# Kernel optimization log

Hardware: AMD Instinct MI355X
Metric: run time of the kernel (lower is better)

Reference implementation:

```python
import jax, jax.numpy as jnp
import numpy as np

N_NODES = 50000
N_EDGES = 800000
N_GRAPHS = 64
IN_DIM = 128
HID = 64
HEADS = 4
LAT = 32
BN_EPS = 1e-5


def setup_inputs() -> dict:
    key = jax.random.key(0)
    ks = jax.random.split(key, 16)
    x = jax.random.normal(ks[0], (N_NODES, IN_DIM), jnp.float32)
    edge_index = jax.random.randint(ks[1], (2, N_EDGES), 0, N_NODES, dtype=jnp.int64)
    batch = jnp.sort(jax.random.randint(ks[2], (N_NODES,), 0, N_GRAPHS, dtype=jnp.int64))

    def lin(k, fan_in, shape):
        return (jax.random.normal(k, shape, jnp.float32) / np.sqrt(fan_in)).astype(jnp.float32)

    d = {"x": x, "edge_index": edge_index, "batch": batch}
    dims = [IN_DIM, HID, HID]
    i = 3
    for l, din in enumerate(dims):
        d[f"Wl{l}"] = lin(ks[i], din, (din, HEADS * HID)); i += 1
        d[f"Wr{l}"] = lin(ks[i], din, (din, HEADS * HID)); i += 1
        d[f"att{l}"] = lin(ks[i], HID, (HEADS, HID)); i += 1
        d[f"b{l}"] = jnp.zeros((HID,), jnp.float32)
    d["bn_gamma"] = jnp.ones((HID,), jnp.float32)
    d["bn_beta"] = jnp.zeros((HID,), jnp.float32)
    d["fc_W"] = lin(ks[i], HID, (LAT, HID)); i += 1
    d["fc_b"] = jnp.zeros((LAT,), jnp.float32)
    return d


def _gatv2_conv(x, Wl, Wr, att, b, src, dst):
    # PyG GATv2Conv, concat=False: mean over heads. src -> dst message flow.
    n = x.shape[0]
    H, D = att.shape
    xl = (x @ Wl).reshape(n, H, D)   # source-side transform
    xr = (x @ Wr).reshape(n, H, D)   # target-side transform
    e = jax.nn.leaky_relu(xl[src] + xr[dst], 0.2)        # [E, H, D]
    logits = jnp.einsum('ehd,hd->eh', e, att)            # [E, H]
    # segment softmax over incoming edges of each dst node
    m = jax.ops.segment_max(logits, dst, num_segments=n)
    p = jnp.exp(logits - m[dst])
    denom = jax.ops.segment_sum(p, dst, num_segments=n)
    alpha = p / (denom[dst] + 1e-16)                     # [E, H]
    out = jax.ops.segment_sum(alpha[..., None] * xl[src], dst, num_segments=n)  # [N, H, D]
    return out.mean(axis=1) + b


def reference(x, edge_index, batch, Wl0, Wr0, att0, b0, Wl1, Wr1, att1, b1,
              Wl2, Wr2, att2, b2, bn_gamma, bn_beta, fc_W, fc_b):
    src, dst = edge_index[0], edge_index[1]
    h = x
    for (Wl, Wr, att, b) in ((Wl0, Wr0, att0, b0), (Wl1, Wr1, att1, b1), (Wl2, Wr2, att2, b2)):
        h = _gatv2_conv(h, Wl, Wr, att, b, src, dst)
        h = jax.nn.leaky_relu(h, 0.1)
        # dropout omitted (deterministic reference / eval semantics)
    pooled = jax.ops.segment_sum(h, batch, num_segments=N_GRAPHS)  # [G, HID]
    mean = pooled.mean(axis=0)
    var = pooled.var(axis=0)  # biased variance, matches BN training normalization
    y = (pooled - mean) / jnp.sqrt(var + BN_EPS) * bn_gamma + bn_beta
    return y @ fc_W.T + fc_b
```

## Files before the change

kernel.cpp:

```cpp
#include <hip/hip_runtime.h>
#include <hip/hip_bf16.h>
#include <math.h>
#include <string.h>

#define N_NODES 50000
#define N_EDGES 800000
#define N_GRAPHS 64
#define IN_DIM 128
#define HID 64
#define HEADS 4
#define LAT 32
#define SCAN_BLOCKS ((N_NODES + 255) / 256)
#define ES_CAP 960000

typedef __attribute__((ext_vector_type(8))) short bf16x8;
typedef __attribute__((ext_vector_type(4))) float floatx4;
typedef __attribute__((ext_vector_type(2))) float f32x2;

__device__ inline unsigned short f2bf(float f) {
    unsigned u = __float_as_uint(f);
    return (unsigned short)((u + 0x7fffu + ((u >> 16) & 1u)) >> 16);
}

__device__ inline unsigned pkbf(float x, float y) {
    float2 f{x, y};
    __hip_bfloat162 h = __float22bfloat162_rn(f);
    unsigned u;
    memcpy(&u, &h, sizeof(u));
    return u;
}

__device__ inline f32x2 bfpair(unsigned u) {
    f32x2 r;
    r.x = __uint_as_float(u << 16);
    r.y = __uint_as_float(u & 0xffff0000u);
    return r;
}

__device__ inline float rowsum16(float x) {
    x += __int_as_float(__builtin_amdgcn_mov_dpp(__float_as_int(x), 0x128, 0xf, 0xf, false));
    x += __int_as_float(__builtin_amdgcn_mov_dpp(__float_as_int(x), 0x124, 0xf, 0xf, false));
    x += __int_as_float(__builtin_amdgcn_mov_dpp(__float_as_int(x), 0x122, 0xf, 0xf, false));
    x += __int_as_float(__builtin_amdgcn_mov_dpp(__float_as_int(x), 0x121, 0xf, 0xf, false));
    return x;
}

__global__ __launch_bounds__(256) void prep_kernel(
    const float* __restrict__ x, unsigned* __restrict__ xbf,
    const float* __restrict__ Wl0, const float* __restrict__ Wr0,
    const float* __restrict__ Wl1, const float* __restrict__ Wr1,
    const float* __restrict__ Wl2, const float* __restrict__ Wr2,
    unsigned short* __restrict__ B0, unsigned short* __restrict__ B1,
    unsigned short* __restrict__ B2,
    int* __restrict__ cnt, float* __restrict__ pooled, int* __restrict__ done,
    uint4* __restrict__ es4) {
    int b = blockIdx.x, t = threadIdx.x;
    if (b < 3072) {
        for (int i = b * 256 + t; i < N_NODES * IN_DIM / 2; i += 3072 * 256) {
            float2 v = reinterpret_cast<const float2*>(x)[i];
            xbf[i] = pkbf(v.x, v.y);
        }
    } else if (b < 3584) {
        int idx = (b - 3072) * 256 + t;
        const float *Wl, *Wr;
        unsigned short* B;
        int KC, local;
        if (idx < 65536)      { Wl = Wl0; Wr = Wr0; B = B0; KC = 4; local = idx; }
        else if (idx < 98304) { Wl = Wl1; Wr = Wr1; B = B1; KC = 2; local = idx - 65536; }
        else                  { Wl = Wl2; Wr = Wr2; B = B2; KC = 2; local = idx - 98304; }
        int j = local & 7;
        int lane = (local >> 3) & 63;
        int rem = local >> 9;
        int kc = rem % KC;
        int tile = rem / KC;
        int k = kc * 32 + (lane >> 4) * 8 + j;
        int tt = tile & 15;
        int n = (tt >> 3) * 128 + (lane & 15) * 8 + (tt & 7);
        const float* W = (tile < 16) ? Wl : Wr;
        B[local] = f2bf(W[k * 256 + n]);
    } else if (b < 3840) {
        int idx = (b - 3584) * 256 + t;
        if (idx < N_NODES) cnt[idx] = 0;
        if (idx < N_GRAPHS * HID) pooled[idx] = 0.f;
        if (idx == 0) *done = 0;
    } else {
        int idx = (b - 3840) * 256 + t;
        for (int i = idx; i < ES_CAP / 4; i += 65536)
            es4[i] = uint4{0, 0, 0, 0};
    }
}

__global__ __launch_bounds__(256) void deg_kernel(const int* __restrict__ dsts,
                                                  int* __restrict__ cnt, int E) {
    int e = blockIdx.x * 256 + threadIdx.x;
    if (e < E) atomicAdd(&cnt[dsts[e]], 1);
}

__global__ __launch_bounds__(256) void scan_kernel(const int* __restrict__ cnt,
                                                   int* __restrict__ offs,
                                                   int* __restrict__ sc,
                                                   int* __restrict__ agg) {
    __shared__ int buf[256];
    int b = blockIdx.x, t = threadIdx.x;
    int i = b * 256 + t;
    int v = (i < N_NODES) ? ((cnt[i] + 3) & ~3) : 0;
    buf[t] = v;
    __syncthreads();
    #pragma unroll
    for (int off = 1; off < 256; off <<= 1) {
        int tmp = (t >= off) ? buf[t - off] : 0;
        __syncthreads();
        buf[t] += tmp;
        __syncthreads();
    }
    int incl = buf[t];
    if (t == 255)
        __hip_atomic_store(&agg[b], buf[255] | 0x40000000,
                           __ATOMIC_RELEASE, __HIP_MEMORY_SCOPE_AGENT);
    int contrib = 0;
    if (t < b) {
        int vv;
        do {
            vv = __hip_atomic_load(&agg[t], __ATOMIC_ACQUIRE, __HIP_MEMORY_SCOPE_AGENT);
        } while (vv < 0 || !(vv & 0x40000000));
        contrib = vv & 0x3FFFFFFF;
    }
    __syncthreads();
    buf[t] = contrib;
    __syncthreads();
    for (int off = 128; off; off >>= 1) {
        if (t < off) buf[t] += buf[t + off];
        __syncthreads();
    }
    if (i < N_NODES) {
        offs[i] = buf[0] + incl - v;
        sc[i] = 0;
    }
}

__global__ __launch_bounds__(256) void scatter_kernel(const int* __restrict__ srcs,
                                                      const int* __restrict__ dsts,
                                                      const int* __restrict__ offs,
                                                      int* __restrict__ sc,
                                                      int* __restrict__ es, int E) {
    int e = blockIdx.x * 256 + threadIdx.x;
    if (e < E) {
        int d = dsts[e];
        int pos = offs[d] + atomicAdd(&sc[d], 1);
        es[pos] = srcs[e];
    }
}

template <int K>
__global__ __launch_bounds__(256) void gemm_mfma_kernel(
    const unsigned short* __restrict__ Abf,
    const unsigned short* __restrict__ Bpk,
    unsigned* __restrict__ xlp_u,
    unsigned* __restrict__ xrp_u) {
    constexpr int KC = K / 32;
    int br = blockIdx.x * 32;
    int t = threadIdx.x;
    int wave = t >> 6, lane = t & 63;
    int quad = lane >> 4, l16 = lane & 15;

    bf16x8 afrag[2][KC];
    #pragma unroll
    for (int rt = 0; rt < 2; ++rt) {
        int row = br + rt * 16 + l16;
        if (row > N_NODES - 1) row = N_NODES - 1;
        const unsigned short* ap = Abf + (size_t)row * K + quad * 8;
        #pragma unroll
        for (int kc = 0; kc < KC; ++kc)
            afrag[rt][kc] = *reinterpret_cast<const bf16x8*>(ap + kc * 32);
    }

    floatx4 acc[2][8];
    #pragma unroll
    for (int rt = 0; rt < 2; ++rt)
        #pragma unroll
        for (int i = 0; i < 8; ++i) acc[rt][i] = floatx4{0.f, 0.f, 0.f, 0.f};

    const bf16x8* bbase = reinterpret_cast<const bf16x8*>(Bpk)
                          + (size_t)(wave * 8) * KC * 64 + lane;
    #pragma unroll
    for (int i = 0; i < 8; ++i) {
        #pragma unroll
        for (int kc = 0; kc < KC; ++kc) {
            bf16x8 bfr = bbase[(i * KC + kc) * 64];
            acc[0][i] = __builtin_amdgcn_mfma_f32_16x16x32_bf16(afrag[0][kc], bfr, acc[0][i], 0, 0, 0);
            acc[1][i] = __builtin_amdgcn_mfma_f32_16x16x32_bf16(afrag[1][kc], bfr, acc[1][i], 0, 0, 0);
        }
    }

    unsigned* dst = (wave < 2) ? xlp_u : xrp_u;
    int cbase = (wave & 1) * 64 + l16 * 4;
    #pragma unroll
    for (int rt = 0; rt < 2; ++rt) {
        if (br + rt * 16 >= N_NODES) break;
        #pragma unroll
        for (int r = 0; r < 4; ++r) {
            int row = br + rt * 16 + quad * 4 + r;
            uint4 pk;
            pk.x = pkbf(acc[rt][0][r], acc[rt][1][r]);
            pk.y = pkbf(acc[rt][2][r], acc[rt][3][r]);
            pk.z = pkbf(acc[rt][4][r], acc[rt][5][r]);
            pk.w = pkbf(acc[rt][6][r], acc[rt][7][r]);
            *reinterpret_cast<uint4*>(&dst[(size_t)row * 128 + cbase]) = pk;
        }
    }
}

__global__ __launch_bounds__(256) void attn_kernel(const unsigned* __restrict__ xlp,
                                                   const unsigned* __restrict__ xrp,
                                                   const int* __restrict__ es,
                                                   const int* __restrict__ offs,
                                                   const int* __restrict__ deg,
                                                   const float4* __restrict__ att4,
                                                   const float4* __restrict__ bias4,
                                                   float* __restrict__ hout,
                                                   unsigned* __restrict__ hbf) {
    int node = blockIdx.x * 4 + (threadIdx.x >> 6);
    int lane = threadIdx.x & 63;
    int beg = offs[node];
    int end = beg + deg[node];
    uint2 xr2 = reinterpret_cast<const uint2*>(xrp)[(size_t)node * 64 + lane];
    f32x2 xrA = bfpair(xr2.x), xrB = bfpair(xr2.y);
    float4 at_t = att4[lane];
    f32x2 atA = {at_t.x, at_t.y}, atB = {at_t.z, at_t.w};
    const char* xbase = (const char*)xlp;
    int laneoff = lane << 3;

    float l = 0.f;
    f32x2 accA = {0.f, 0.f}, accB = {0.f, 0.f};

    auto edge_z = [&](uint2 v, f32x2& xa, f32x2& xb) -> float {
        xa = bfpair(v.x);
        xb = bfpair(v.y);
        f32x2 ea = xa + xrA;
        f32x2 eb = xb + xrB;
        ea = __builtin_elementwise_max(ea, ea * 0.2f);
        eb = __builtin_elementwise_max(eb, eb * 0.2f);
        f32x2 zz = ea * atA;
        zz += eb * atB;
        return zz.x + zz.y;
    };
    auto gather = [&](int s) -> uint2 {
        return *reinterpret_cast<const uint2*>(
            xbase + (((size_t)(unsigned)s) << 9) + laneoff);
    };

    for (int cb = beg; cb < end; cb += 4) {
        int4 s4 = *reinterpret_cast<const int4*>(&es[cb]);
        uint2 v0 = gather(s4.x);
        uint2 v1 = gather(s4.y);
        uint2 v2 = gather(s4.z);
        uint2 v3 = gather(s4.w);
        f32x2 xa0, xb0, xa1, xb1, xa2, xb2, xa3, xb3;
        float z0 = rowsum16(edge_z(v0, xa0, xb0));
        float z1 = rowsum16(edge_z(v1, xa1, xb1));
        float z2 = rowsum16(edge_z(v2, xa2, xb2));
        float z3 = rowsum16(edge_z(v3, xa3, xb3));
        float p0 = __expf(z0);
        float p1 = (cb + 1 < end) ? __expf(z1) : 0.f;
        float p2 = (cb + 2 < end) ? __expf(z2) : 0.f;
        float p3 = (cb + 3 < end) ? __expf(z3) : 0.f;
        accA += p0 * xa0 + p1 * xa1 + p2 * xa2 + p3 * xa3;
        accB += p0 * xb0 + p1 * xb1 + p2 * xb2 + p3 * xb3;
        l += (p0 + p1) + (p2 + p3);
    }

    float inv = 1.f / (l + 1e-16f);
    float a0 = accA.x * inv, a1 = accA.y * inv;
    float a2 = accB.x * inv, a3 = accB.y * inv;
    a0 += __shfl_xor(a0, 16); a0 += __shfl_xor(a0, 32);
    a1 += __shfl_xor(a1, 16); a1 += __shfl_xor(a1, 32);
    a2 += __shfl_xor(a2, 16); a2 += __shfl_xor(a2, 32);
    a3 += __shfl_xor(a3, 16); a3 += __shfl_xor(a3, 32);
    if (lane < 16) {
        float4 bv = bias4[lane];
        float4 o;
        o.x = 0.25f * a0 + bv.x; o.x = (o.x > 0.f) ? o.x : 0.1f * o.x;
        o.y = 0.25f * a1 + bv.y; o.y = (o.y > 0.f) ? o.y : 0.1f * o.y;
        o.z = 0.25f * a2 + bv.z; o.z = (o.z > 0.f) ? o.z : 0.1f * o.z;
        o.w = 0.25f * a3 + bv.w; o.w = (o.w > 0.f) ? o.w : 0.1f * o.w;
        if (hout)
            *reinterpret_cast<float4*>(&hout[(size_t)node * HID + lane * 4]) = o;
        if (hbf) {
            uint2 pk;
            pk.x = pkbf(o.x, o.y);
            pk.y = pkbf(o.z, o.w);
            *reinterpret_cast<uint2*>(&hbf[(size_t)node * 32 + lane * 2]) = pk;
        }
    }
}

__global__ __launch_bounds__(256) void pool_final_kernel(
    const float* __restrict__ hfin, const int* __restrict__ batch,
    float* __restrict__ pooled,
    const float* __restrict__ gamma, const float* __restrict__ beta,
    const float* __restrict__ fcW, const float* __restrict__ fcb,
    float* __restrict__ out, int* __restrict__ done) {
    int base = blockIdx.x * 256;
    int g = threadIdx.x >> 6, lane = threadIdx.x & 63;
    int lim = min(base + 256, N_NODES);
    int cur = -1;
    float s = 0.f;
    for (int i = base + g; i < lim; i += 4) {
        int b = batch[i];
        if (b != cur) {
            if (cur >= 0) atomicAdd(&pooled[cur * HID + lane], s);
            cur = b; s = 0.f;
        }
        s += hfin[(size_t)i * HID + lane];
    }
    if (cur >= 0) atomicAdd(&pooled[cur * HID + lane], s);

    __threadfence();
    __syncthreads();
    __shared__ int lastS;
    if (threadIdx.x == 0)
        lastS = (atomicAdd(done, 1) == (int)gridDim.x - 1);
    __syncthreads();
    if (!lastS) return;

    __shared__ float P[N_GRAPHS * HID];
    __shared__ float normS[N_GRAPHS * HID];
    __shared__ float meanS[HID], rstdS[HID];
    int t = threadIdx.x;
    for (int i = t; i < N_GRAPHS * HID; i += 256)
        P[i] = __hip_atomic_load(&pooled[i], __ATOMIC_RELAXED, __HIP_MEMORY_SCOPE_AGENT);
    __syncthreads();
    if (t < HID) {
        float s2 = 0.f;
        for (int g2 = 0; g2 < N_GRAPHS; ++g2) s2 += P[g2 * HID + t];
        float mean = s2 / (float)N_GRAPHS;
        float v = 0.f;
        for (int g2 = 0; g2 < N_GRAPHS; ++g2) {
            float dd = P[g2 * HID + t] - mean;
            v += dd * dd;
        }
        v /= (float)N_GRAPHS;
        meanS[t] = mean;
        rstdS[t] = rsqrtf(v + 1e-5f);
    }
    __syncthreads();
    for (int i = t; i < N_GRAPHS * HID; i += 256) {
        int d = i & 63;
        normS[i] = (P[i] - meanS[d]) * rstdS[d] * gamma[d] + beta[d];
    }
    __syncthreads();
    for (int i = t; i < N_GRAPHS * LAT; i += 256) {
        int g2 = i >> 5, lat = i & 31;
        float s2 = fcb[lat];
        for (int d = 0; d < HID; ++d) s2 += normS[g2 * HID + d] * fcW[lat * HID + d];
        out[i] = s2;
    }
}

extern "C" void kernel_launch(void* const* d_in, const int* in_sizes, int n_in,
                              void* d_out, int out_size, void* d_ws, size_t ws_size,
                              hipStream_t stream) {
    const float* x      = (const float*)d_in[0];
    const int*   ei     = (const int*)d_in[1];
    const int*   batch  = (const int*)d_in[2];
    const float* Wl[3]  = {(const float*)d_in[3], (const float*)d_in[7],  (const float*)d_in[11]};
    const float* Wr[3]  = {(const float*)d_in[4], (const float*)d_in[8],  (const float*)d_in[12]};
    const float* att[3] = {(const float*)d_in[5], (const float*)d_in[9],  (const float*)d_in[13]};
    const float* bia[3] = {(const float*)d_in[6], (const float*)d_in[10], (const float*)d_in[14]};
    const float* gamma  = (const float*)d_in[15];
    const float* beta   = (const float*)d_in[16];
    const float* fcW    = (const float*)d_in[17];
    const float* fcb    = (const float*)d_in[18];
    float* out = (float*)d_out;

    char* p = (char*)d_ws;
    auto alloc = [&](size_t bytes) {
        char* r = p;
        p += (bytes + 255) & ~(size_t)255;
        return r;
    };
    unsigned* xbf   = (unsigned*)alloc((size_t)N_NODES * IN_DIM * 2);
    unsigned* xlp   = (unsigned*)alloc((size_t)N_NODES * 256 * 2);
    unsigned* xrp   = (unsigned*)alloc((size_t)N_NODES * 256 * 2);
    unsigned* hbf0  = (unsigned*)alloc((size_t)N_NODES * HID * 2);
    unsigned* hbf1  = (unsigned*)alloc((size_t)N_NODES * HID * 2);
    unsigned short* Bpk0 = (unsigned short*)alloc(32 * 4 * 512 * 2);
    unsigned short* Bpk1 = (unsigned short*)alloc(32 * 2 * 512 * 2);
    unsigned short* Bpk2 = (unsigned short*)alloc(32 * 2 * 512 * 2);
    int*   es      = (int*)alloc((size_t)ES_CAP * 4);
    int*   offs    = (int*)alloc((size_t)N_NODES * 4);
    int*   cnt     = (int*)alloc((size_t)N_NODES * 4);
    int*   sc      = (int*)alloc((size_t)N_NODES * 4);
    int*   agg     = (int*)alloc((size_t)SCAN_BLOCKS * 4);
    int*   done    = (int*)alloc(256);
    float* pooled  = (float*)alloc((size_t)N_GRAPHS * HID * 4);
    float* hfin    = (float*)xbf;

    const int* srcs = ei;
    const int* dsts = ei + N_EDGES;

    prep_kernel<<<4096, 256, 0, stream>>>(x, xbf, Wl[0], Wr[0], Wl[1], Wr[1],
                                          Wl[2], Wr[2], Bpk0, Bpk1, Bpk2,
                                          cnt, pooled, done, (uint4*)es);
    int eb = (N_EDGES + 255) / 256;
    deg_kernel<<<eb, 256, 0, stream>>>(dsts, cnt, N_EDGES);
    scan_kernel<<<SCAN_BLOCKS, 256, 0, stream>>>(cnt, offs, sc, agg);
    scatter_kernel<<<eb, 256, 0, stream>>>(srcs, dsts, offs, sc, es, N_EDGES);

    int gb = (N_NODES + 31) / 32;
    gemm_mfma_kernel<IN_DIM><<<gb, 256, 0, stream>>>((const unsigned short*)xbf, Bpk0, xlp, xrp);
    attn_kernel<<<N_NODES / 4, 256, 0, stream>>>(xlp, xrp, es, offs, cnt,
                                                 (const float4*)att[0],
                                                 (const float4*)bia[0], nullptr, hbf0);
    gemm_mfma_kernel<HID><<<gb, 256, 0, stream>>>((const unsigned short*)hbf0, Bpk1, xlp, xrp);
    attn_kernel<<<N_NODES / 4, 256, 0, stream>>>(xlp, xrp, es, offs, cnt,
                                                 (const float4*)att[1],
                                                 (const float4*)bia[1], nullptr, hbf1);
    gemm_mfma_kernel<HID><<<gb, 256, 0, stream>>>((const unsigned short*)hbf1, Bpk2, xlp, xrp);
    attn_kernel<<<N_NODES / 4, 256, 0, stream>>>(xlp, xrp, es, offs, cnt,
                                                 (const float4*)att[2],
                                                 (const float4*)bia[2], hfin, nullptr);

    pool_final_kernel<<<SCAN_BLOCKS, 256, 0, stream>>>(hfin, batch, pooled,
                                                       gamma, beta, fcW, fcb,
                                                       out, done);
}
```

Baseline: 500.3 us.

## Stage GEMM A tile in LDS with 64-row blocks and vectorize edge kernels

The GEMM now processes 64 rows per 512-thread block, staging the A tile in shared memory so each wave reuses four row-tiles per B fragment load. The B packing and output column mapping change to match. Separately, the degree and scatter kernels read four edges per thread through int4 loads. This cuts redundant B-fragment global loads and per-edge load overhead, at the cost of more LDS use, a barrier, and more accumulator registers per thread.

After: 486.9 us. 2.7% less time.

```diff
diff --git a/kernel.cpp b/kernel.cpp
--- a/kernel.cpp
+++ b/kernel.cpp
@@ -75,7 +75,7 @@
         int tile = rem / KC;
         int k = kc * 32 + (lane >> 4) * 8 + j;
         int tt = tile & 15;
-        int n = (tt >> 3) * 128 + (lane & 15) * 8 + (tt & 7);
+        int n = (tt >> 2) * 64 + (lane & 15) * 4 + (tt & 3);
         const float* W = (tile < 16) ? Wl : Wr;
         B[local] = f2bf(W[k * 256 + n]);
     } else if (b < 3840) {
@@ -90,10 +90,16 @@
     }
 }
 
-__global__ __launch_bounds__(256) void deg_kernel(const int* __restrict__ dsts,
-                                                  int* __restrict__ cnt, int E) {
-    int e = blockIdx.x * 256 + threadIdx.x;
-    if (e < E) atomicAdd(&cnt[dsts[e]], 1);
+__global__ __launch_bounds__(256) void deg_kernel(const int4* __restrict__ dsts4,
+                                                  int* __restrict__ cnt, int E4) {
+    int i = blockIdx.x * 256 + threadIdx.x;
+    if (i < E4) {
+        int4 d = dsts4[i];
+        atomicAdd(&cnt[d.x], 1);
+        atomicAdd(&cnt[d.y], 1);
+        atomicAdd(&cnt[d.z], 1);
+        atomicAdd(&cnt[d.w], 1);
+    }
 }
 
 __global__ __launch_bounds__(256) void scan_kernel(const int* __restrict__ cnt,
@@ -138,74 +144,90 @@
     }
 }
 
-__global__ __launch_bounds__(256) void scatter_kernel(const int* __restrict__ srcs,
-                                                      const int* __restrict__ dsts,
+__global__ __launch_bounds__(256) void scatter_kernel(const int4* __restrict__ srcs4,
+                                                      const int4* __restrict__ dsts4,
                                                       const int* __restrict__ offs,
                                                       int* __restrict__ sc,
-                                                      int* __restrict__ es, int E) {
-    int e = blockIdx.x * 256 + threadIdx.x;
-    if (e < E) {
-        int d = dsts[e];
-        int pos = offs[d] + atomicAdd(&sc[d], 1);
-        es[pos] = srcs[e];
+                                                      int* __restrict__ es, int E4) {
+    int i = blockIdx.x * 256 + threadIdx.x;
+    if (i < E4) {
+        int4 s = srcs4[i];
+        int4 d = dsts4[i];
+        es[offs[d.x] + atomicAdd(&sc[d.x], 1)] = s.x;
+        es[offs[d.y] + atomicAdd(&sc[d.y], 1)] = s.y;
+        es[offs[d.z] + atomicAdd(&sc[d.z], 1)] = s.z;
+        es[offs[d.w] + atomicAdd(&sc[d.w], 1)] = s.w;
     }
 }
 
 template <int K>
-__global__ __launch_bounds__(256) void gemm_mfma_kernel(
+__global__ __launch_bounds__(512) void gemm_mfma_kernel(
     const unsigned short* __restrict__ Abf,
     const unsigned short* __restrict__ Bpk,
     unsigned* __restrict__ xlp_u,
     unsigned* __restrict__ xrp_u) {
     constexpr int KC = K / 32;
-    int br = blockIdx.x * 32;
+    constexpr int CHUNKS = 64 * K / 8;
+    __shared__ short As[CHUNKS * 8];
+    int br = blockIdx.x * 64;
     int t = threadIdx.x;
+
+    for (int c = t; c < CHUNKS; c += 512) {
+        int rt = c / (KC * 64);
+        int rem = c % (KC * 64);
+        int kc = rem >> 6;
+        int quad = (rem >> 4) & 3, l16 = rem & 15;
+        int row = br + rt * 16 + l16;
+        if (row >= N_NODES) row = N_NODES - 1;
+        *reinterpret_cast<uint4*>(&As[c * 8]) =
+            *reinterpret_cast<const uint4*>(&Abf[(size_t)row * K + kc * 32 + quad * 8]);
+    }
+    __syncthreads();
+
     int wave = t >> 6, lane = t & 63;
     int quad = lane >> 4, l16 = lane & 15;
-
-    bf16x8 afrag[2][KC];
+    int which = wave >> 2, g = wave & 3;
+
+    bf16x8 afrag[4][KC];
     #pragma unroll
-    for (int rt = 0; rt < 2; ++rt) {
-        int row = br + rt * 16 + l16;
-        if (row > N_NODES - 1) row = N_NODES - 1;
-        const unsigned short* ap = Abf + (size_t)row * K + quad * 8;
+    for (int rt = 0; rt < 4; ++rt)
         #pragma unroll
         for (int kc = 0; kc < KC; ++kc)
-            afrag[rt][kc] = *reinterpret_cast<const bf16x8*>(ap + kc * 32);
-    }
-
-    floatx4 acc[2][8];
+            afrag[rt][kc] = *reinterpret_cast<const bf16x8*>(
+                &As[(((rt * KC + kc) * 4 + quad) * 16 + l16) * 8]);
+
+    floatx4 acc[4][4];
     #pragma unroll
-    for (int rt = 0; rt < 2; ++rt)
+    for (int rt = 0; rt < 4; ++rt)
         #pragma unroll
-        for (int i = 0; i < 8; ++i) acc[rt][i] = floatx4{0.f, 0.f, 0.f, 0.f};
-
-    const bf16x8* bbase = reinterpret_cast<const bf16x8*>(Bpk)
-                          + (size_t)(wave * 8) * KC * 64 + lane;
+        for (int i = 0; i < 4; ++i) acc[rt][i] = floatx4{0.f, 0.f, 0.f, 0.f};
+
     #pragma unroll
-    for (int i = 0; i < 8; ++i) {
+    for (int i = 0; i < 4; ++i) {
+        int T = which * 16 + g * 4 + i;
         #pragma unroll
         for (int kc = 0; kc < KC; ++kc) {
-            bf16x8 bfr = bbase[(i * KC + kc) * 64];
-            acc[0][i] = __builtin_amdgcn_mfma_f32_16x16x32_bf16(afrag[0][kc], bfr, acc[0][i], 0, 0, 0);
-            acc[1][i] = __builtin_amdgcn_mfma_f32_16x16x32_bf16(afrag[1][kc], bfr, acc[1][i], 0, 0, 0);
-        }
-    }
-
-    unsigned* dst = (wave < 2) ? xlp_u : xrp_u;
-    int cbase = (wave & 1) * 64 + l16 * 4;
+            bf16x8 bfr = *reinterpret_cast<const bf16x8*>(
+                &Bpk[(size_t)((T * KC + kc) * 64 + lane) * 8]);
+            #pragma unroll
+            for (int rt = 0; rt < 4; ++rt)
+                acc[rt][i] = __builtin_amdgcn_mfma_f32_16x16x32_bf16(
+                    afrag[rt][kc], bfr, acc[rt][i], 0, 0, 0);
+        }
+    }
+
+    unsigned* dst = which ? xrp_u : xlp_u;
+    int dcol = g * 32 + l16 * 2;
     #pragma unroll
-    for (int rt = 0; rt < 2; ++rt) {
-        if (br + rt * 16 >= N_NODES) break;
+    for (int rt = 0; rt < 4; ++rt) {
         #pragma unroll
         for (int r = 0; r < 4; ++r) {
             int row = br + rt * 16 + quad * 4 + r;
-            uint4 pk;
+            if (row >= N_NODES) continue;
+            uint2 pk;
             pk.x = pkbf(acc[rt][0][r], acc[rt][1][r]);
             pk.y = pkbf(acc[rt][2][r], acc[rt][3][r]);
-            pk.z = pkbf(acc[rt][4][r], acc[rt][5][r]);
-            pk.w = pkbf(acc[rt][6][r], acc[rt][7][r]);
-            *reinterpret_cast<uint4*>(&dst[(size_t)row * 128 + cbase]) = pk;
+            *reinterpret_cast<uint2*>(&dst[(size_t)row * 128 + dcol]) = pk;
         }
     }
 }
@@ -402,21 +424,23 @@
     prep_kernel<<<4096, 256, 0, stream>>>(x, xbf, Wl[0], Wr[0], Wl[1], Wr[1],
                                           Wl[2], Wr[2], Bpk0, Bpk1, Bpk2,
                                           cnt, pooled, done, (uint4*)es);
-    int eb = (N_EDGES + 255) / 256;
-    deg_kernel<<<eb, 256, 0, stream>>>(dsts, cnt, N_EDGES);
+    int e4 = N_EDGES / 4;
+    int eb4 = (e4 + 255) / 256;
+    deg_kernel<<<eb4, 256, 0, stream>>>((const int4*)dsts, cnt, e4);
     scan_kernel<<<SCAN_BLOCKS, 256, 0, stream>>>(cnt, offs, sc, agg);
-    scatter_kernel<<<eb, 256, 0, stream>>>(srcs, dsts, offs, sc, es, N_EDGES);
-
-    int gb = (N_NODES + 31) / 32;
-    gemm_mfma_kernel<IN_DIM><<<gb, 256, 0, stream>>>((const unsigned short*)xbf, Bpk0, xlp, xrp);
+    scatter_kernel<<<eb4, 256, 0, stream>>>((const int4*)srcs, (const int4*)dsts,
+                                            offs, sc, es, e4);
+
+    int gb = (N_NODES + 63) / 64;
+    gemm_mfma_kernel<IN_DIM><<<gb, 512, 0, stream>>>((const unsigned short*)xbf, Bpk0, xlp, xrp);
     attn_kernel<<<N_NODES / 4, 256, 0, stream>>>(xlp, xrp, es, offs, cnt,
                                                  (const float4*)att[0],
                                                  (const float4*)bia[0], nullptr, hbf0);
-    gemm_mfma_kernel<HID><<<gb, 256, 0, stream>>>((const unsigned short*)hbf0, Bpk1, xlp, xrp);
+    gemm_mfma_kernel<HID><<<gb, 512, 0, stream>>>((const unsigned short*)hbf0, Bpk1, xlp, xrp);
     attn_kernel<<<N_NODES / 4, 256, 0, stream>>>(xlp, xrp, es, offs, cnt,
                                                  (const float4*)att[1],
                                                  (const float4*)bia[1], nullptr, hbf1);
-    gemm_mfma_kernel<HID><<<gb, 256, 0, stream>>>((const unsigned short*)hbf1, Bpk2, xlp, xrp);
+    gemm_mfma_kernel<HID><<<gb, 512, 0, stream>>>((const unsigned short*)hbf1, Bpk2, xlp, xrp);
     attn_kernel<<<N_NODES / 4, 256, 0, stream>>>(xlp, xrp, es, offs, cnt,
                                                  (const float4*)att[2],
                                                  (const float4*)bia[2], hfin, nullptr);
```
